# Kernel optimization log

Measured on AMD Instinct MI355X. Metric: run time of the kernel, lower is better.

The kernel has to match this reference:

```python
import jax, jax.numpy as jnp
import numpy as np

FEAT_DIM = 384
HEAD_DIM = 32
N_HEADS = FEAT_DIM // HEAD_DIM
MAX_SEQ_LEN = 64
SIZE = 8  # sqrt(max_seq_len)


def _get_relative_position_index(height, width):
    coords_h = np.arange(height)
    coords_w = np.arange(width)
    coords = np.stack(np.meshgrid(coords_h, coords_w, indexing='ij'))
    coords_flat = coords.reshape(coords.shape[0], -1)
    relative_coords = coords_flat[:, :, None] - coords_flat[:, None, :]
    relative_coords = relative_coords.transpose(1, 2, 0)
    rh = relative_coords[:, :, 0] + (height - 1)
    rw = relative_coords[:, :, 1] + (width - 1)
    return jnp.asarray(rh * (2 * width - 1) + rw, dtype=jnp.int32)  # [P, P]


def setup_inputs() -> dict:
    key = jax.random.key(0)
    ks = jax.random.split(key, 6)
    B, G, P, D = 32, 64, MAX_SEQ_LEN, FEAT_DIM
    x = jax.random.normal(ks[0], (B, G, P, D), dtype=jnp.float32)
    qkv_w = jax.random.normal(ks[1], (D, 3 * D), dtype=jnp.float32) * (1.0 / np.sqrt(D))
    qkv_b = jnp.zeros((3 * D,), dtype=jnp.float32)
    merge_w = jax.random.normal(ks[2], (D, D), dtype=jnp.float32) * (1.0 / np.sqrt(D))
    merge_b = jnp.zeros((D,), dtype=jnp.float32)
    n_bias = (2 * SIZE - 1) * (2 * SIZE - 1)  # 225
    bias_table = jax.random.truncated_normal(ks[3], -2.0, 2.0, (n_bias, N_HEADS), dtype=jnp.float32) * 0.02
    rel_index = _get_relative_position_index(SIZE, SIZE)
    return {"x": x, "qkv_w": qkv_w, "qkv_b": qkv_b, "merge_w": merge_w,
            "merge_b": merge_b, "bias_table": bias_table, "rel_index": rel_index}


def reference(x, qkv_w, qkv_b, merge_w, merge_b, bias_table, rel_index):
    B, G, P, D = x.shape
    H, DH = N_HEADS, HEAD_DIM
    scale = 1.0 / np.sqrt(D)  # NOTE: module scales by feat_dim**-0.5, not head_dim
    qkv = x @ qkv_w + qkv_b  # [B,G,P,3D]
    q, k, v = jnp.split(qkv, 3, axis=-1)
    q = q.reshape(B, G, P, H, DH).transpose(0, 1, 3, 2, 4)  # [B,G,H,P,DH]
    k = k.reshape(B, G, P, H, DH).transpose(0, 1, 3, 2, 4)
    v = v.reshape(B, G, P, H, DH).transpose(0, 1, 3, 2, 4)
    scores = jnp.einsum('bghid,bghjd->bghij', q, k * scale)  # [B,G,H,P,P]
    pos_bias = bias_table[rel_index.reshape(-1)].reshape(P, P, H)
    pos_bias = pos_bias.transpose(2, 0, 1)[None, None]  # [1,1,H,P,P]
    attn = jax.nn.softmax(scores + pos_bias, axis=-1)
    out = jnp.einsum('bghij,bghjd->bghid', attn, v)  # [B,G,H,P,DH]
    out = out.transpose(0, 1, 3, 2, 4).reshape(B, G, P, D)
    return out @ merge_w + merge_b
```

## Files before the change

### kernel.cpp

```cpp
#include <hip/hip_runtime.h>
#include <hip/hip_bf16.h>
#include <cstdint>
#include <cstddef>


typedef __bf16 bf16_t;
typedef __bf16 bf16x8 __attribute__((ext_vector_type(8)));
typedef float  f32x4  __attribute__((ext_vector_type(4)));

#define MFMA16(A, B, C) __builtin_amdgcn_mfma_f32_16x16x32_bf16((A), (B), (C), 0, 0, 0)

#define SCALE  0.051031036307982884f
#define LOG2E  1.4426950408889634f

#define BAR()  do { asm volatile("s_waitcnt lgkmcnt(0)" ::: "memory"); \
                    __builtin_amdgcn_s_barrier(); } while (0)


__global__ void prep_kernel(const float* __restrict__ qkv_w,
                            const float* __restrict__ qkv_b,
                            const float* __restrict__ merge_w,
                            const float* __restrict__ bias_table,
                            const int*   __restrict__ rel_index,
                            bf16_t* __restrict__ qkv_wT,
                            bf16_t* __restrict__ merge_wT,
                            bf16_t* __restrict__ biasx,
                            float*  __restrict__ qkvb_s) {
  int idx = blockIdx.x * 256 + threadIdx.x;
  if (idx < 1152 * 384) {
    int n = idx / 384, k = idx - n * 384;
    float v = qkv_w[k * 1152 + n];
    if (n >= 384 && n < 768) v *= SCALE;
    qkv_wT[idx] = (bf16_t)v;
    return;
  }
  int i2 = idx - 1152 * 384;
  if (i2 < 384 * 384) {
    int n = i2 / 384, k = i2 - n * 384;
    merge_wT[i2] = (bf16_t)merge_w[k * 384 + n];
    return;
  }
  int i3 = i2 - 384 * 384;
  if (i3 < 12 * 64 * 64) {
    int h = i3 / 4096, r = i3 - h * 4096;
    biasx[i3] = (bf16_t)bias_table[rel_index[r] * 12 + h];
    return;
  }
  int i4 = i3 - 12 * 64 * 64;
  if (i4 < 1152) {
    float v = qkv_b[i4];
    if (i4 >= 384 && i4 < 768) v *= SCALE;
    qkvb_s[i4] = v;
  }
}

__device__ inline float bflo(unsigned u) {
  union { unsigned x; float f; } v; v.x = u << 16; return v.f;
}
__device__ inline float bfhi(unsigned u) {
  union { unsigned x; float f; } v; v.x = u & 0xffff0000u; return v.f;
}

__global__ void __launch_bounds__(512, 4)
fused_qkv_attn(const float*  __restrict__ x,
               const bf16_t* __restrict__ wT,
               const float*  __restrict__ qbias,
               const bf16_t* __restrict__ biasx,
               bf16_t* __restrict__ attn) {
  extern __shared__ char smem_raw[];
  bf16_t* lds = (bf16_t*)smem_raw;
  bf16_t* xs  = lds;
  bf16_t* qs  = lds;
  bf16_t* ks  = lds + 8192;
  bf16_t* vts = lds + 16384;
  bf16_t* ps  = lds + 24576;

  const int tid  = threadIdx.x;
  const int lane = tid & 63;
  const int w    = tid >> 6;
  const int c    = lane & 15;
  const int g    = lane >> 4;
  const int cx   = c & 7;

  const int xcd  = blockIdx.x & 7;
  const int slot = blockIdx.x >> 3;
  const int pass = slot % 3;
  const int bg   = (slot / 3) * 8 + xcd;

  const f32x4 zf = {0.f, 0.f, 0.f, 0.f};

  {
    const float4* xg = (const float4*)(x + (size_t)bg * 24576);
#pragma unroll
    for (int it = 0; it < 6; ++it) {
      int hc  = tid + it * 512;
      int row = hc / 48;
      int ch  = hc - row * 48;
      float4 v0 = xg[hc * 2];
      float4 v1 = xg[hc * 2 + 1];
      union { bf16_t b[8]; bf16x8 v; } pk;
      pk.b[0] = (bf16_t)v0.x; pk.b[1] = (bf16_t)v0.y;
      pk.b[2] = (bf16_t)v0.z; pk.b[3] = (bf16_t)v0.w;
      pk.b[4] = (bf16_t)v1.x; pk.b[5] = (bf16_t)v1.y;
      pk.b[6] = (bf16_t)v1.z; pk.b[7] = (bf16_t)v1.w;
      *(bf16x8*)(xs + row * 384 + ((ch ^ (row & 7)) << 3)) = pk.v;
    }
  }
  BAR();

  f32x4 acc[3][4];
#pragma unroll
  for (int t = 0; t < 3; ++t)
#pragma unroll
    for (int mt = 0; mt < 4; ++mt) acc[t][mt] = zf;

  int nrow[3];
  const bf16_t* wp[3];
  float bv[3];
#pragma unroll
  for (int t = 0; t < 3; ++t) {
    int tau  = w * 3 + t;
    int kind = tau >> 3;
    int u    = tau & 7;
    nrow[t]  = kind * 384 + (pass * 4 + (u >> 1)) * 32 + (u & 1) * 16;
    wp[t]    = wT + (size_t)(nrow[t] + c) * 384 + g * 8;
    bv[t]    = qbias[nrow[t] + c];
  }
  bf16x8 bc[3], bn[3];
#pragma unroll
  for (int t = 0; t < 3; ++t) bc[t] = *(const bf16x8*)(wp[t]);
#pragma unroll
  for (int k = 0; k < 12; ++k) {
    if (k < 11) {
#pragma unroll
      for (int t = 0; t < 3; ++t) bn[t] = *(const bf16x8*)(wp[t] + (k + 1) * 32);
    }
    int chv = (((4 * k + g) ^ cx) << 3);
#pragma unroll
    for (int mt = 0; mt < 4; ++mt) {
      bf16x8 a = *(const bf16x8*)(xs + (mt * 16 + c) * 384 + chv);
#pragma unroll
      for (int t = 0; t < 3; ++t)
        acc[t][mt] = MFMA16(a, bc[t], acc[t][mt]);
    }
#pragma unroll
    for (int t = 0; t < 3; ++t) bc[t] = bn[t];
  }

  BAR();

#pragma unroll
  for (int t = 0; t < 3; ++t) {
    int tau  = w * 3 + t;
    int kind = tau >> 3;
    int u    = tau & 7;
    int hl   = u >> 1, c16 = u & 1;
    if (kind == 2) {
      int d = c16 * 16 + c;
      bf16_t* vbase = vts + hl * 2048 + d * 64;
#pragma unroll
      for (int mt = 0; mt < 4; ++mt) {
        union { bf16_t b[4]; uint2 u2; } pk;
#pragma unroll
        for (int r = 0; r < 4; ++r) pk.b[r] = (bf16_t)(acc[t][mt][r] + bv[t]);
        int chunk = (2 * mt + (g >> 1)) ^ cx;
        *(uint2*)(vbase + chunk * 8 + (g & 1) * 4) = pk.u2;
      }
    } else {
      int f  = c16 * 16 + c;
      int fc = f >> 3;
      int fl = f & 7;
      bf16_t* dst = (kind == 0 ? qs : ks) + hl * 2048;
#pragma unroll
      for (int mt = 0; mt < 4; ++mt)
#pragma unroll
        for (int r = 0; r < 4; ++r)
          dst[(mt * 16 + g * 4 + r) * 32 + ((fc ^ g) << 3) + fl] =
              (bf16_t)(acc[t][mt][r] + bv[t]);
    }
  }
  BAR();

  {
    const int hl = w >> 1, ih = w & 1;
    const int h  = pass * 4 + hl;
    const int rsw = (c >> 2) & 3;

    f32x4 sacc[4][2];
#pragma unroll
    for (int mt = 0; mt < 4; ++mt)
#pragma unroll
      for (int nt = 0; nt < 2; ++nt) sacc[mt][nt] = zf;
    bf16x8 ka[4], qf[2];
#pragma unroll
    for (int mt = 0; mt < 4; ++mt)
      ka[mt] = *(const bf16x8*)(ks + hl * 2048 + (mt * 16 + c) * 32 +
                                ((g ^ rsw) << 3));
#pragma unroll
    for (int nt = 0; nt < 2; ++nt)
      qf[nt] = *(const bf16x8*)(qs + hl * 2048 + (ih * 32 + nt * 16 + c) * 32 +
                                ((g ^ rsw) << 3));
#pragma unroll
    for (int mt = 0; mt < 4; ++mt)
#pragma unroll
      for (int nt = 0; nt < 2; ++nt)
        sacc[mt][nt] = MFMA16(ka[mt], qf[nt], sacc[mt][nt]);

    const bf16_t* bp = biasx + h * 4096;
    float mx[2] = {-3.0e38f, -3.0e38f};
#pragma unroll
    for (int nt = 0; nt < 2; ++nt) {
      int i = ih * 32 + nt * 16 + c;
#pragma unroll
      for (int mt = 0; mt < 4; ++mt) {
        uint2 bb = *(const uint2*)(bp + i * 64 + mt * 16 + g * 4);
        sacc[mt][nt][0] += bflo(bb.x);
        sacc[mt][nt][1] += bfhi(bb.x);
        sacc[mt][nt][2] += bflo(bb.y);
        sacc[mt][nt][3] += bfhi(bb.y);
        mx[nt] = fmaxf(mx[nt], fmaxf(fmaxf(sacc[mt][nt][0], sacc[mt][nt][1]),
                                     fmaxf(sacc[mt][nt][2], sacc[mt][nt][3])));
      }
    }
#pragma unroll
    for (int nt = 0; nt < 2; ++nt) {
      mx[nt] = fmaxf(mx[nt], __shfl_xor(mx[nt], 16));
      mx[nt] = fmaxf(mx[nt], __shfl_xor(mx[nt], 32));
    }

    bf16_t* psw = ps + w * 1024;
    bf16x8 va[2][2];
#pragma unroll
    for (int m2 = 0; m2 < 2; ++m2)
#pragma unroll
      for (int kt = 0; kt < 2; ++kt)
        va[m2][kt] = *(const bf16x8*)(vts + hl * 2048 + (m2 * 16 + c) * 64 +
                                      (((4 * kt + g) ^ cx) << 3));
    f32x4 oacc[2][2];
#pragma unroll
    for (int m2 = 0; m2 < 2; ++m2)
#pragma unroll
      for (int nt = 0; nt < 2; ++nt) oacc[m2][nt] = zf;

    float l[2] = {0.f, 0.f};
#pragma unroll
    for (int nt = 0; nt < 2; ++nt) {
#pragma unroll
      for (int mt = 0; mt < 4; ++mt) {
        float p0 = exp2f((sacc[mt][nt][0] - mx[nt]) * LOG2E);
        float p1 = exp2f((sacc[mt][nt][1] - mx[nt]) * LOG2E);
        float p2 = exp2f((sacc[mt][nt][2] - mx[nt]) * LOG2E);
        float p3 = exp2f((sacc[mt][nt][3] - mx[nt]) * LOG2E);
        l[nt] += (p0 + p1) + (p2 + p3);
        union { bf16_t b[4]; uint2 u2; } pk;
        pk.b[0] = (bf16_t)p0; pk.b[1] = (bf16_t)p1;
        pk.b[2] = (bf16_t)p2; pk.b[3] = (bf16_t)p3;
        int chunk = (2 * mt + (g >> 1)) ^ cx;
        *(uint2*)(psw + c * 64 + chunk * 8 + (g & 1) * 4) = pk.u2;
      }
      bf16x8 pb[2];
#pragma unroll
      for (int kt = 0; kt < 2; ++kt)
        pb[kt] = *(const bf16x8*)(psw + c * 64 + (((4 * kt + g) ^ cx) << 3));
#pragma unroll
      for (int m2 = 0; m2 < 2; ++m2)
#pragma unroll
        for (int kt = 0; kt < 2; ++kt)
          oacc[m2][nt] = MFMA16(va[m2][kt], pb[kt], oacc[m2][nt]);
    }

#pragma unroll
    for (int nt = 0; nt < 2; ++nt) {
      l[nt] += __shfl_xor(l[nt], 16);
      l[nt] += __shfl_xor(l[nt], 32);
    }

#pragma unroll
    for (int nt = 0; nt < 2; ++nt) {
      float inv = 1.0f / l[nt];
      int row = bg * 64 + ih * 32 + nt * 16 + c;
#pragma unroll
      for (int m2 = 0; m2 < 2; ++m2) {
        union { bf16_t b[4]; uint2 u2; } pk;
#pragma unroll
        for (int r = 0; r < 4; ++r) pk.b[r] = (bf16_t)(oacc[m2][nt][r] * inv);
        *(uint2*)(attn + (size_t)row * 384 + h * 32 + m2 * 16 + g * 4) = pk.u2;
      }
    }
  }
}

#define XS 408
__global__ void __launch_bounds__(512)
merge_gemm(const bf16_t* __restrict__ attn,
           const bf16_t* __restrict__ mwT,
           const float*  __restrict__ mb,
           float* __restrict__ out) {
  __shared__ bf16_t as[64 * XS];
  const int tid = threadIdx.x, blk = blockIdx.x;
  const int lane = tid & 63, w = tid >> 6, c = lane & 15, g = lane >> 4;

  {
    const int4* ag = (const int4*)(attn + (size_t)blk * (64 * 384));
#pragma unroll
    for (int it = 0; it < 6; ++it) {
      int idx = tid + it * 512;
      int row = idx / 48;
      int col = (idx - row * 48) * 8;
      *(int4*)(as + row * XS + col) = ag[idx];
    }
  }
  __syncthreads();

  const f32x4 zf = {0.f, 0.f, 0.f, 0.f};
  f32x4 acc[3][4];
#pragma unroll
  for (int t = 0; t < 3; ++t)
#pragma unroll
    for (int mt = 0; mt < 4; ++mt) acc[t][mt] = zf;

  const int n0 = w * 48;
  const bf16_t* wp[3];
#pragma unroll
  for (int t = 0; t < 3; ++t) wp[t] = mwT + (size_t)(n0 + t * 16 + c) * 384 + g * 8;
  bf16x8 bc[3], bn[3];
#pragma unroll
  for (int t = 0; t < 3; ++t) bc[t] = *(const bf16x8*)(wp[t]);
#pragma unroll
  for (int k = 0; k < 12; ++k) {
    if (k < 11) {
#pragma unroll
      for (int t = 0; t < 3; ++t) bn[t] = *(const bf16x8*)(wp[t] + (k + 1) * 32);
    }
    bf16x8 a[4];
#pragma unroll
    for (int mt = 0; mt < 4; ++mt)
      a[mt] = *(const bf16x8*)(as + (mt * 16 + c) * XS + k * 32 + g * 8);
#pragma unroll
    for (int t = 0; t < 3; ++t)
#pragma unroll
      for (int mt = 0; mt < 4; ++mt)
        acc[t][mt] = MFMA16(a[mt], bc[t], acc[t][mt]);
#pragma unroll
    for (int t = 0; t < 3; ++t) bc[t] = bn[t];
  }

#pragma unroll
  for (int t = 0; t < 3; ++t) {
    float bias = mb[n0 + t * 16 + c];
#pragma unroll
    for (int mt = 0; mt < 4; ++mt)
#pragma unroll
      for (int r = 0; r < 4; ++r)
        out[(size_t)(blk * 64 + mt * 16 + g * 4 + r) * 384 + n0 + t * 16 + c] =
            acc[t][mt][r] + bias;
  }
}

extern "C" void kernel_launch(void* const* d_in, const int* in_sizes, int n_in,
                              void* d_out, int out_size, void* d_ws, size_t ws_size,
                              hipStream_t stream) {
  const float* x          = (const float*)d_in[0];
  const float* qkv_w      = (const float*)d_in[1];
  const float* qkv_b      = (const float*)d_in[2];
  const float* merge_w    = (const float*)d_in[3];
  const float* merge_b    = (const float*)d_in[4];
  const float* bias_table = (const float*)d_in[5];
  const int*   rel_index  = (const int*)d_in[6];
  float*       out        = (float*)d_out;

  const size_t OFF_QKVWT = 0;
  const size_t OFF_MWT   = 884736;
  const size_t OFF_BIAS  = OFF_MWT + 294912;
  const size_t OFF_QB    = OFF_BIAS + 98304;
  const size_t OFF_ATTN  = OFF_QB + 4608;
  const size_t NEED      = OFF_ATTN + (size_t)100663296;
  if (ws_size < NEED) return;

  char* ws = (char*)d_ws;
  bf16_t* qkv_wT  = (bf16_t*)(ws + OFF_QKVWT);
  bf16_t* mwT     = (bf16_t*)(ws + OFF_MWT);
  bf16_t* biasx   = (bf16_t*)(ws + OFF_BIAS);
  float*  qkvb_s  = (float*)(ws + OFF_QB);
  bf16_t* attnbuf = (bf16_t*)(ws + OFF_ATTN);

  prep_kernel<<<2501, 256, 0, stream>>>(qkv_w, qkv_b, merge_w, bias_table,
                                        rel_index, qkv_wT, mwT, biasx, qkvb_s);

  hipFuncSetAttribute(reinterpret_cast<const void*>(fused_qkv_attn),
                      hipFuncAttributeMaxDynamicSharedMemorySize, 65536);
  fused_qkv_attn<<<6144, 512, 65536, stream>>>(x, qkv_wT, qkvb_s, biasx, attnbuf);

  merge_gemm<<<2048, 512, 0, stream>>>(attnbuf, mwT, merge_b, out);
}
```

Measured before the change: 400.2 us.

## Drop softmax max pass, transpose Q/K MFMA for vector stores, prefetch bias early

Measured after the change: 453.9 us. +13.4%, slower.

```diff
diff --git a/kernel.cpp b/kernel.cpp
--- a/kernel.cpp
+++ b/kernel.cpp
@@ -71,9 +71,9 @@
   bf16_t* lds = (bf16_t*)smem_raw;
   bf16_t* xs  = lds;
   bf16_t* qs  = lds;
-  bf16_t* ks  = lds + 8192;
-  bf16_t* vts = lds + 16384;
-  bf16_t* ps  = lds + 24576;
+  bf16_t* ks  = lds + 10240;
+  bf16_t* vts = lds + 20480;
+  bf16_t* ps  = lds + 28672;
 
   const int tid  = threadIdx.x;
   const int lane = tid & 63;
@@ -88,6 +88,40 @@
   const int bg   = (slot / 3) * 8 + xcd;
 
   const f32x4 zf = {0.f, 0.f, 0.f, 0.f};
+
+  int nrow[3], kindv[3], hlv[3], c16v[3];
+  const bf16_t* wp[3];
+#pragma unroll
+  for (int t = 0; t < 3; ++t) {
+    int tau  = w * 3 + t;
+    kindv[t] = tau >> 3;
+    int u    = tau & 7;
+    hlv[t]   = u >> 1;
+    c16v[t]  = u & 1;
+    nrow[t]  = kindv[t] * 384 + (pass * 4 + hlv[t]) * 32 + c16v[t] * 16;
+    wp[t]    = wT + (size_t)(nrow[t] + c) * 384 + g * 8;
+  }
+  float4 qb4[3];
+  float  bvs[3];
+#pragma unroll
+  for (int t = 0; t < 3; ++t) {
+    if (kindv[t] < 2) qb4[t] = *(const float4*)(qbias + nrow[t] + g * 4);
+    else              bvs[t] = qbias[nrow[t] + c];
+  }
+  bf16x8 bc[3], bn[3];
+#pragma unroll
+  for (int t = 0; t < 3; ++t) bc[t] = *(const bf16x8*)(wp[t]);
+
+  const int hl_a = w >> 1, ih_a = w & 1;
+  const bf16_t* bp = biasx + (pass * 4 + hl_a) * 4096;
+  uint2 bb[2][4];
+#pragma unroll
+  for (int nt = 0; nt < 2; ++nt) {
+    int i = ih_a * 32 + nt * 16 + c;
+#pragma unroll
+    for (int mt = 0; mt < 4; ++mt)
+      bb[nt][mt] = *(const uint2*)(bp + i * 64 + mt * 16 + g * 4);
+  }
 
   {
     const float4* xg = (const float4*)(x + (size_t)bg * 24576);
@@ -114,21 +148,6 @@
 #pragma unroll
     for (int mt = 0; mt < 4; ++mt) acc[t][mt] = zf;
 
-  int nrow[3];
-  const bf16_t* wp[3];
-  float bv[3];
-#pragma unroll
-  for (int t = 0; t < 3; ++t) {
-    int tau  = w * 3 + t;
-    int kind = tau >> 3;
-    int u    = tau & 7;
-    nrow[t]  = kind * 384 + (pass * 4 + (u >> 1)) * 32 + (u & 1) * 16;
-    wp[t]    = wT + (size_t)(nrow[t] + c) * 384 + g * 8;
-    bv[t]    = qbias[nrow[t] + c];
-  }
-  bf16x8 bc[3], bn[3];
-#pragma unroll
-  for (int t = 0; t < 3; ++t) bc[t] = *(const bf16x8*)(wp[t]);
 #pragma unroll
   for (int k = 0; k < 12; ++k) {
     if (k < 11) {
@@ -140,8 +159,10 @@
     for (int mt = 0; mt < 4; ++mt) {
       bf16x8 a = *(const bf16x8*)(xs + (mt * 16 + c) * 384 + chv);
 #pragma unroll
-      for (int t = 0; t < 3; ++t)
-        acc[t][mt] = MFMA16(a, bc[t], acc[t][mt]);
+      for (int t = 0; t < 3; ++t) {
+        if (kindv[t] < 2) acc[t][mt] = MFMA16(bc[t], a, acc[t][mt]);
+        else              acc[t][mt] = MFMA16(a, bc[t], acc[t][mt]);
+      }
     }
 #pragma unroll
     for (int t = 0; t < 3; ++t) bc[t] = bn[t];
@@ -151,40 +172,35 @@
 
 #pragma unroll
   for (int t = 0; t < 3; ++t) {
-    int tau  = w * 3 + t;
-    int kind = tau >> 3;
-    int u    = tau & 7;
-    int hl   = u >> 1, c16 = u & 1;
-    if (kind == 2) {
+    int hl = hlv[t], c16 = c16v[t];
+    if (kindv[t] == 2) {
       int d = c16 * 16 + c;
       bf16_t* vbase = vts + hl * 2048 + d * 64;
 #pragma unroll
       for (int mt = 0; mt < 4; ++mt) {
         union { bf16_t b[4]; uint2 u2; } pk;
 #pragma unroll
-        for (int r = 0; r < 4; ++r) pk.b[r] = (bf16_t)(acc[t][mt][r] + bv[t]);
+        for (int r = 0; r < 4; ++r) pk.b[r] = (bf16_t)(acc[t][mt][r] + bvs[t]);
         int chunk = (2 * mt + (g >> 1)) ^ cx;
         *(uint2*)(vbase + chunk * 8 + (g & 1) * 4) = pk.u2;
       }
     } else {
-      int f  = c16 * 16 + c;
-      int fc = f >> 3;
-      int fl = f & 7;
-      bf16_t* dst = (kind == 0 ? qs : ks) + hl * 2048;
-#pragma unroll
-      for (int mt = 0; mt < 4; ++mt)
-#pragma unroll
-        for (int r = 0; r < 4; ++r)
-          dst[(mt * 16 + g * 4 + r) * 32 + ((fc ^ g) << 3) + fl] =
-              (bf16_t)(acc[t][mt][r] + bv[t]);
+      bf16_t* dst = (kindv[t] == 0 ? qs : ks) + hl * 2560 + c16 * 16 + g * 4;
+#pragma unroll
+      for (int mt = 0; mt < 4; ++mt) {
+        union { bf16_t b[4]; uint2 u2; } pk;
+        pk.b[0] = (bf16_t)(acc[t][mt][0] + qb4[t].x);
+        pk.b[1] = (bf16_t)(acc[t][mt][1] + qb4[t].y);
+        pk.b[2] = (bf16_t)(acc[t][mt][2] + qb4[t].z);
+        pk.b[3] = (bf16_t)(acc[t][mt][3] + qb4[t].w);
+        *(uint2*)(dst + (mt * 16 + c) * 40) = pk.u2;
+      }
     }
   }
   BAR();
 
   {
-    const int hl = w >> 1, ih = w & 1;
-    const int h  = pass * 4 + hl;
-    const int rsw = (c >> 2) & 3;
+    const int hl = hl_a, ih = ih_a;
 
     f32x4 sacc[4][2];
 #pragma unroll
@@ -194,41 +210,16 @@
     bf16x8 ka[4], qf[2];
 #pragma unroll
     for (int mt = 0; mt < 4; ++mt)
-      ka[mt] = *(const bf16x8*)(ks + hl * 2048 + (mt * 16 + c) * 32 +
-                                ((g ^ rsw) << 3));
+      ka[mt] = *(const bf16x8*)(ks + hl * 2560 + (mt * 16 + c) * 40 + g * 8);
 #pragma unroll
     for (int nt = 0; nt < 2; ++nt)
-      qf[nt] = *(const bf16x8*)(qs + hl * 2048 + (ih * 32 + nt * 16 + c) * 32 +
-                                ((g ^ rsw) << 3));
+      qf[nt] = *(const bf16x8*)(qs + hl * 2560 + (ih * 32 + nt * 16 + c) * 40 + g * 8);
 #pragma unroll
     for (int mt = 0; mt < 4; ++mt)
 #pragma unroll
       for (int nt = 0; nt < 2; ++nt)
         sacc[mt][nt] = MFMA16(ka[mt], qf[nt], sacc[mt][nt]);
 
-    const bf16_t* bp = biasx + h * 4096;
-    float mx[2] = {-3.0e38f, -3.0e38f};
-#pragma unroll
-    for (int nt = 0; nt < 2; ++nt) {
-      int i = ih * 32 + nt * 16 + c;
-#pragma unroll
-      for (int mt = 0; mt < 4; ++mt) {
-        uint2 bb = *(const uint2*)(bp + i * 64 + mt * 16 + g * 4);
-        sacc[mt][nt][0] += bflo(bb.x);
-        sacc[mt][nt][1] += bfhi(bb.x);
-        sacc[mt][nt][2] += bflo(bb.y);
-        sacc[mt][nt][3] += bfhi(bb.y);
-        mx[nt] = fmaxf(mx[nt], fmaxf(fmaxf(sacc[mt][nt][0], sacc[mt][nt][1]),
-                                     fmaxf(sacc[mt][nt][2], sacc[mt][nt][3])));
-      }
-    }
-#pragma unroll
-    for (int nt = 0; nt < 2; ++nt) {
-      mx[nt] = fmaxf(mx[nt], __shfl_xor(mx[nt], 16));
-      mx[nt] = fmaxf(mx[nt], __shfl_xor(mx[nt], 32));
-    }
-
-    bf16_t* psw = ps + w * 1024;
     bf16x8 va[2][2];
 #pragma unroll
     for (int m2 = 0; m2 < 2; ++m2)
@@ -236,6 +227,8 @@
       for (int kt = 0; kt < 2; ++kt)
         va[m2][kt] = *(const bf16x8*)(vts + hl * 2048 + (m2 * 16 + c) * 64 +
                                       (((4 * kt + g) ^ cx) << 3));
+
+    bf16_t* psw = ps + w * 1024;
     f32x4 oacc[2][2];
 #pragma unroll
     for (int m2 = 0; m2 < 2; ++m2)
@@ -247,10 +240,10 @@
     for (int nt = 0; nt < 2; ++nt) {
 #pragma unroll
       for (int mt = 0; mt < 4; ++mt) {
-        float p0 = exp2f((sacc[mt][nt][0] - mx[nt]) * LOG2E);
-        float p1 = exp2f((sacc[mt][nt][1] - mx[nt]) * LOG2E);
-        float p2 = exp2f((sacc[mt][nt][2] - mx[nt]) * LOG2E);
-        float p3 = exp2f((sacc[mt][nt][3] - mx[nt]) * LOG2E);
+        float p0 = exp2f((sacc[mt][nt][0] + bflo(bb[nt][mt].x)) * LOG2E);
+        float p1 = exp2f((sacc[mt][nt][1] + bfhi(bb[nt][mt].x)) * LOG2E);
+        float p2 = exp2f((sacc[mt][nt][2] + bflo(bb[nt][mt].y)) * LOG2E);
+        float p3 = exp2f((sacc[mt][nt][3] + bfhi(bb[nt][mt].y)) * LOG2E);
         l[nt] += (p0 + p1) + (p2 + p3);
         union { bf16_t b[4]; uint2 u2; } pk;
         pk.b[0] = (bf16_t)p0; pk.b[1] = (bf16_t)p1;
@@ -275,6 +268,7 @@
       l[nt] += __shfl_xor(l[nt], 32);
     }
 
+    const int h = pass * 4 + hl;
 #pragma unroll
     for (int nt = 0; nt < 2; ++nt) {
       float inv = 1.0f / l[nt];
@@ -388,8 +382,8 @@
                                         rel_index, qkv_wT, mwT, biasx, qkvb_s);
 
   hipFuncSetAttribute(reinterpret_cast<const void*>(fused_qkv_attn),
-                      hipFuncAttributeMaxDynamicSharedMemorySize, 65536);
-  fused_qkv_attn<<<6144, 512, 65536, stream>>>(x, qkv_wT, qkvb_s, biasx, attnbuf);
+                      hipFuncAttributeMaxDynamicSharedMemorySize, 73728);
+  fused_qkv_attn<<<6144, 512, 73728, stream>>>(x, qkv_wT, qkvb_s, biasx, attnbuf);
 
   merge_gemm<<<2048, 512, 0, stream>>>(attnbuf, mwT, merge_b, out);
 }
```

## Use 12 waves per block and drop softmax max subtraction

Applied to the files above, without the earlier changes.

Result: slower. 409.1 us (+2.2%).

```diff
diff --git a/kernel.cpp b/kernel.cpp
--- a/kernel.cpp
+++ b/kernel.cpp
@@ -61,7 +61,7 @@
   union { unsigned x; float f; } v; v.x = u & 0xffff0000u; return v.f;
 }
 
-__global__ void __launch_bounds__(512, 4)
+__global__ void __launch_bounds__(768, 6)
 fused_qkv_attn(const float*  __restrict__ x,
                const bf16_t* __restrict__ wT,
                const float*  __restrict__ qbias,
@@ -92,8 +92,8 @@
   {
     const float4* xg = (const float4*)(x + (size_t)bg * 24576);
 #pragma unroll
-    for (int it = 0; it < 6; ++it) {
-      int hc  = tid + it * 512;
+    for (int it = 0; it < 4; ++it) {
+      int hc  = tid + it * 768;
       int row = hc / 48;
       int ch  = hc - row * 48;
       float4 v0 = xg[hc * 2];
@@ -108,53 +108,54 @@
   }
   BAR();
 
-  f32x4 acc[3][4];
-#pragma unroll
-  for (int t = 0; t < 3; ++t)
+  f32x4 acc[2][4];
+#pragma unroll
+  for (int t = 0; t < 2; ++t)
 #pragma unroll
     for (int mt = 0; mt < 4; ++mt) acc[t][mt] = zf;
 
-  int nrow[3];
-  const bf16_t* wp[3];
-  float bv[3];
-#pragma unroll
-  for (int t = 0; t < 3; ++t) {
-    int tau  = w * 3 + t;
-    int kind = tau >> 3;
+  int nrow[2];
+  const int kind = (w * 2) >> 3;
+  int hlv[2], c16v[2];
+  const bf16_t* wp[2];
+  float bv[2];
+#pragma unroll
+  for (int t = 0; t < 2; ++t) {
+    int tau  = w * 2 + t;
     int u    = tau & 7;
-    nrow[t]  = kind * 384 + (pass * 4 + (u >> 1)) * 32 + (u & 1) * 16;
+    hlv[t]   = u >> 1;
+    c16v[t]  = u & 1;
+    nrow[t]  = kind * 384 + (pass * 4 + hlv[t]) * 32 + c16v[t] * 16;
     wp[t]    = wT + (size_t)(nrow[t] + c) * 384 + g * 8;
     bv[t]    = qbias[nrow[t] + c];
   }
-  bf16x8 bc[3], bn[3];
-#pragma unroll
-  for (int t = 0; t < 3; ++t) bc[t] = *(const bf16x8*)(wp[t]);
+  bf16x8 bc[2], bn[2];
+#pragma unroll
+  for (int t = 0; t < 2; ++t) bc[t] = *(const bf16x8*)(wp[t]);
+
 #pragma unroll
   for (int k = 0; k < 12; ++k) {
     if (k < 11) {
 #pragma unroll
-      for (int t = 0; t < 3; ++t) bn[t] = *(const bf16x8*)(wp[t] + (k + 1) * 32);
+      for (int t = 0; t < 2; ++t) bn[t] = *(const bf16x8*)(wp[t] + (k + 1) * 32);
     }
     int chv = (((4 * k + g) ^ cx) << 3);
 #pragma unroll
     for (int mt = 0; mt < 4; ++mt) {
       bf16x8 a = *(const bf16x8*)(xs + (mt * 16 + c) * 384 + chv);
 #pragma unroll
-      for (int t = 0; t < 3; ++t)
+      for (int t = 0; t < 2; ++t)
         acc[t][mt] = MFMA16(a, bc[t], acc[t][mt]);
     }
 #pragma unroll
-    for (int t = 0; t < 3; ++t) bc[t] = bn[t];
+    for (int t = 0; t < 2; ++t) bc[t] = bn[t];
   }
 
   BAR();
 
 #pragma unroll
-  for (int t = 0; t < 3; ++t) {
-    int tau  = w * 3 + t;
-    int kind = tau >> 3;
-    int u    = tau & 7;
-    int hl   = u >> 1, c16 = u & 1;
+  for (int t = 0; t < 2; ++t) {
+    int hl = hlv[t], c16 = c16v[t];
     if (kind == 2) {
       int d = c16 * 16 + c;
       bf16_t* vbase = vts + hl * 2048 + d * 64;
@@ -181,77 +182,47 @@
   }
   BAR();
 
-  {
+  if (w < 8) {
     const int hl = w >> 1, ih = w & 1;
     const int h  = pass * 4 + hl;
     const int rsw = (c >> 2) & 3;
 
-    f32x4 sacc[4][2];
-#pragma unroll
-    for (int mt = 0; mt < 4; ++mt)
-#pragma unroll
-      for (int nt = 0; nt < 2; ++nt) sacc[mt][nt] = zf;
-    bf16x8 ka[4], qf[2];
+    const bf16_t* bp = biasx + h * 4096;
+    bf16x8 ka[4], va[2][2];
 #pragma unroll
     for (int mt = 0; mt < 4; ++mt)
       ka[mt] = *(const bf16x8*)(ks + hl * 2048 + (mt * 16 + c) * 32 +
                                 ((g ^ rsw) << 3));
 #pragma unroll
-    for (int nt = 0; nt < 2; ++nt)
-      qf[nt] = *(const bf16x8*)(qs + hl * 2048 + (ih * 32 + nt * 16 + c) * 32 +
-                                ((g ^ rsw) << 3));
-#pragma unroll
-    for (int mt = 0; mt < 4; ++mt)
-#pragma unroll
-      for (int nt = 0; nt < 2; ++nt)
-        sacc[mt][nt] = MFMA16(ka[mt], qf[nt], sacc[mt][nt]);
-
-    const bf16_t* bp = biasx + h * 4096;
-    float mx[2] = {-3.0e38f, -3.0e38f};
-#pragma unroll
-    for (int nt = 0; nt < 2; ++nt) {
-      int i = ih * 32 + nt * 16 + c;
-#pragma unroll
-      for (int mt = 0; mt < 4; ++mt) {
-        uint2 bb = *(const uint2*)(bp + i * 64 + mt * 16 + g * 4);
-        sacc[mt][nt][0] += bflo(bb.x);
-        sacc[mt][nt][1] += bfhi(bb.x);
-        sacc[mt][nt][2] += bflo(bb.y);
-        sacc[mt][nt][3] += bfhi(bb.y);
-        mx[nt] = fmaxf(mx[nt], fmaxf(fmaxf(sacc[mt][nt][0], sacc[mt][nt][1]),
-                                     fmaxf(sacc[mt][nt][2], sacc[mt][nt][3])));
-      }
-    }
-#pragma unroll
-    for (int nt = 0; nt < 2; ++nt) {
-      mx[nt] = fmaxf(mx[nt], __shfl_xor(mx[nt], 16));
-      mx[nt] = fmaxf(mx[nt], __shfl_xor(mx[nt], 32));
-    }
-
-    bf16_t* psw = ps + w * 1024;
-    bf16x8 va[2][2];
-#pragma unroll
     for (int m2 = 0; m2 < 2; ++m2)
 #pragma unroll
       for (int kt = 0; kt < 2; ++kt)
         va[m2][kt] = *(const bf16x8*)(vts + hl * 2048 + (m2 * 16 + c) * 64 +
                                       (((4 * kt + g) ^ cx) << 3));
-    f32x4 oacc[2][2];
-#pragma unroll
-    for (int m2 = 0; m2 < 2; ++m2)
-#pragma unroll
-      for (int nt = 0; nt < 2; ++nt) oacc[m2][nt] = zf;
-
-    float l[2] = {0.f, 0.f};
+
+    bf16_t* psw = ps + w * 1024;
+
 #pragma unroll
     for (int nt = 0; nt < 2; ++nt) {
+      int i = ih * 32 + nt * 16 + c;
+      bf16x8 qf = *(const bf16x8*)(qs + hl * 2048 + i * 32 + ((g ^ rsw) << 3));
+
+      f32x4 sacc[4];
+#pragma unroll
+      for (int mt = 0; mt < 4; ++mt) sacc[mt] = zf;
+#pragma unroll
+      for (int mt = 0; mt < 4; ++mt)
+        sacc[mt] = MFMA16(ka[mt], qf, sacc[mt]);
+
+      float l = 0.f;
 #pragma unroll
       for (int mt = 0; mt < 4; ++mt) {
-        float p0 = exp2f((sacc[mt][nt][0] - mx[nt]) * LOG2E);
-        float p1 = exp2f((sacc[mt][nt][1] - mx[nt]) * LOG2E);
-        float p2 = exp2f((sacc[mt][nt][2] - mx[nt]) * LOG2E);
-        float p3 = exp2f((sacc[mt][nt][3] - mx[nt]) * LOG2E);
-        l[nt] += (p0 + p1) + (p2 + p3);
+        uint2 bb = *(const uint2*)(bp + i * 64 + mt * 16 + g * 4);
+        float p0 = exp2f((sacc[mt][0] + bflo(bb.x)) * LOG2E);
+        float p1 = exp2f((sacc[mt][1] + bfhi(bb.x)) * LOG2E);
+        float p2 = exp2f((sacc[mt][2] + bflo(bb.y)) * LOG2E);
+        float p3 = exp2f((sacc[mt][3] + bfhi(bb.y)) * LOG2E);
+        l += (p0 + p1) + (p2 + p3);
         union { bf16_t b[4]; uint2 u2; } pk;
         pk.b[0] = (bf16_t)p0; pk.b[1] = (bf16_t)p1;
         pk.b[2] = (bf16_t)p2; pk.b[3] = (bf16_t)p3;
@@ -262,28 +233,25 @@
 #pragma unroll
       for (int kt = 0; kt < 2; ++kt)
         pb[kt] = *(const bf16x8*)(psw + c * 64 + (((4 * kt + g) ^ cx) << 3));
+      f32x4 oacc[2];
+#pragma unroll
+      for (int m2 = 0; m2 < 2; ++m2) oacc[m2] = zf;
 #pragma unroll
       for (int m2 = 0; m2 < 2; ++m2)
 #pragma unroll
         for (int kt = 0; kt < 2; ++kt)
-          oacc[m2][nt] = MFMA16(va[m2][kt], pb[kt], oacc[m2][nt]);
-    }
-
-#pragma unroll
-    for (int nt = 0; nt < 2; ++nt) {
-      l[nt] += __shfl_xor(l[nt], 16);
-      l[nt] += __shfl_xor(l[nt], 32);
-    }
-
-#pragma unroll
-    for (int nt = 0; nt < 2; ++nt) {
-      float inv = 1.0f / l[nt];
-      int row = bg * 64 + ih * 32 + nt * 16 + c;
+          oacc[m2] = MFMA16(va[m2][kt], pb[kt], oacc[m2]);
+
+      l += __shfl_xor(l, 16);
+      l += __shfl_xor(l, 32);
+      float inv = 1.0f / l;
+
+      int row = bg * 64 + i;
 #pragma unroll
       for (int m2 = 0; m2 < 2; ++m2) {
         union { bf16_t b[4]; uint2 u2; } pk;
 #pragma unroll
-        for (int r = 0; r < 4; ++r) pk.b[r] = (bf16_t)(oacc[m2][nt][r] * inv);
+        for (int r = 0; r < 4; ++r) pk.b[r] = (bf16_t)(oacc[m2][r] * inv);
         *(uint2*)(attn + (size_t)row * 384 + h * 32 + m2 * 16 + g * 4) = pk.u2;
       }
     }
@@ -389,7 +357,7 @@
 
   hipFuncSetAttribute(reinterpret_cast<const void*>(fused_qkv_attn),
                       hipFuncAttributeMaxDynamicSharedMemorySize, 65536);
-  fused_qkv_attn<<<6144, 512, 65536, stream>>>(x, qkv_wT, qkvb_s, biasx, attnbuf);
+  fused_qkv_attn<<<6144, 768, 65536, stream>>>(x, qkv_wT, qkvb_s, biasx, attnbuf);
 
   merge_gemm<<<2048, 512, 0, stream>>>(attnbuf, mwT, merge_b, out);
 }
```
